# Performance work log

Measured on AMD Instinct MI355X. Metric: run time of the kernel, lower is better.

Reference implementation:

```python
import jax, jax.numpy as jnp
import numpy as np

B, S, V, D = 64, 1024, 1024, 512


def setup_inputs() -> dict:
    key = jax.random.key(0)
    ks = jax.random.split(key, 18)
    sd = 1.0 / np.sqrt(D)
    return dict(
        map_memory=jnp.zeros((B, S, V), jnp.float32),
        step_memory=jnp.zeros((B, S, S), jnp.float32),
        evidence=jax.random.normal(ks[0], (B, D), jnp.float32),
        marker_id=jax.random.randint(ks[1], (B,), 0, 4, jnp.int32),
        source_idx=jax.random.randint(ks[2], (B,), 0, S, jnp.int32),
        source_mask=jax.random.randint(ks[3], (B,), 0, 2, jnp.int32).astype(bool),
        target_symbol_idx=jax.random.randint(ks[4], (B,), 0, S, jnp.int32),
        target_symbol_mask=jax.random.randint(ks[5], (B,), 0, 2, jnp.int32).astype(bool),
        target_value_idx=jax.random.randint(ks[6], (B,), 0, V, jnp.int32),
        target_value_mask=jax.random.randint(ks[7], (B,), 0, 2, jnp.int32).astype(bool),
        map_W1=jax.random.normal(ks[8], (D, D), jnp.float32) * sd,
        map_b1=jnp.zeros((D,), jnp.float32),
        map_W2=jax.random.normal(ks[9], (D, 1), jnp.float32) * sd,
        map_b2=jnp.zeros((1,), jnp.float32),
        step_W1=jax.random.normal(ks[10], (D, D), jnp.float32) * sd,
        step_b1=jnp.zeros((D,), jnp.float32),
        step_W2=jax.random.normal(ks[11], (D, 1), jnp.float32) * sd,
        step_b2=jnp.zeros((1,), jnp.float32),
    )


def _gain(x, W1, b1, W2, b2):
    # Dense -> gelu (flax default: approximate) -> Dense(1)
    h = jax.nn.gelu(x @ W1 + b1)
    return (h @ W2 + b2)[:, 0]  # [B]


def reference(map_memory, step_memory, evidence, marker_id, source_idx,
              source_mask, target_symbol_idx, target_symbol_mask,
              target_value_idx, target_value_mask,
              map_W1, map_b1, map_W2, map_b2,
              step_W1, step_b1, step_W2, step_b2):
    map_gate = jax.nn.sigmoid(_gain(evidence, map_W1, map_b1, map_W2, map_b2))    # [B]
    step_gate = jax.nn.sigmoid(_gain(evidence, step_W1, step_b1, step_W2, step_b2))  # [B]
    map_mask = ((marker_id == 1) | (marker_id == 2)) & source_mask & target_value_mask
    step_mask = (marker_id == 3) & source_mask & target_symbol_mask
    b = jnp.arange(map_memory.shape[0])
    # one-hot outer product 'bs,bv->bsv' * gate is exactly a single gated entry at
    # (source_idx, target_idx) per batch element -> indexed scatter-add.
    next_map = map_memory.at[b, source_idx, target_value_idx].add(
        map_gate * map_mask.astype(map_gate.dtype))
    next_step = step_memory.at[b, source_idx, target_symbol_idx].add(
        step_gate * step_mask.astype(step_gate.dtype))
    return next_map, next_step
```

## Files before the change

### kernel.cpp

```cpp
#include <hip/hip_runtime.h>
#include <math.h>

#define BB 64
#define SS 1024
#define VV 1024
#define DD 512

#define MAP_WORDS  ((size_t)BB * SS * VV)
#define STEP_WORDS ((size_t)BB * SS * SS)
#define TOT_WORDS  (MAP_WORDS + STEP_WORDS)
#define TOT_F4     (TOT_WORDS / 4)
#define MAP_F4     (MAP_WORDS / 4)

#define COPY_BLOCKS 4096
#define COPY_THREADS 256

typedef float f32x4 __attribute__((ext_vector_type(4)));

__device__ __forceinline__ float gelu_tanh(float x) {
    const float k = 0.7978845608028654f;
    float x3 = x * x * x;
    return 0.5f * x * (1.0f + tanhf(k * (x + 0.044715f * x3)));
}

__global__ void __launch_bounds__(COPY_THREADS)
copy_kernel(const f32x4* __restrict__ map_memory,
            const f32x4* __restrict__ step_memory,
            f32x4* __restrict__ out)
{
    const size_t stride = (size_t)COPY_BLOCKS * COPY_THREADS;
    size_t i = (size_t)blockIdx.x * COPY_THREADS + threadIdx.x;
    for (; i < MAP_F4; i += stride) {
        f32x4 v = __builtin_nontemporal_load(&map_memory[i]);
        __builtin_nontemporal_store(v, &out[i]);
    }
    for (i = (size_t)blockIdx.x * COPY_THREADS + threadIdx.x;
         i < (TOT_F4 - MAP_F4); i += stride) {
        f32x4 v = __builtin_nontemporal_load(&step_memory[i]);
        __builtin_nontemporal_store(v, &out[MAP_F4 + i]);
    }
}

__global__ void __launch_bounds__(256)
gate_scatter_kernel(
    const float* __restrict__ evidence,
    const int* __restrict__ marker_id,
    const int* __restrict__ source_idx,
    const int* __restrict__ source_mask,
    const int* __restrict__ target_symbol_idx,
    const int* __restrict__ target_symbol_mask,
    const int* __restrict__ target_value_idx,
    const int* __restrict__ target_value_mask,
    const float* __restrict__ map_W1, const float* __restrict__ map_b1,
    const float* __restrict__ map_W2, const float* __restrict__ map_b2,
    const float* __restrict__ step_W1, const float* __restrict__ step_b1,
    const float* __restrict__ step_W2, const float* __restrict__ step_b2,
    float* __restrict__ out)
{
    const int b    = blockIdx.x >> 1;
    const int head = blockIdx.x & 1;
    const float* W1  = head ? step_W1 : map_W1;
    const float* b1  = head ? step_b1 : map_b1;
    const float* W2  = head ? step_W2 : map_W2;
    const float* b2v = head ? step_b2 : map_b2;

    __shared__ float ev[DD];
    __shared__ float wsum[4];

    const int tid = threadIdx.x;
    for (int i = tid; i < DD; i += 256) ev[i] = evidence[b * DD + i];
    __syncthreads();

    float acc = 0.0f;
    #pragma unroll
    for (int jj = 0; jj < DD; jj += 256) {
        const int j = jj + tid;
        float h = b1[j];
        for (int k = 0; k < DD; ++k) {
            h = fmaf(ev[k], W1[k * DD + j], h);
        }
        h = gelu_tanh(h);
        acc = fmaf(h, W2[j], acc);
    }

    #pragma unroll
    for (int off = 32; off > 0; off >>= 1) acc += __shfl_down(acc, off, 64);
    if ((tid & 63) == 0) wsum[tid >> 6] = acc;
    __syncthreads();

    if (tid == 0) {
        float g = wsum[0] + wsum[1] + wsum[2] + wsum[3] + b2v[0];
        g = 1.0f / (1.0f + expf(-g));
        const int m  = marker_id[b];
        const bool sm = source_mask[b] != 0;
        if (head == 0) {
            if (((m == 1) || (m == 2)) && sm && (target_value_mask[b] != 0)) {
                size_t idx = (size_t)b * SS * VV + (size_t)source_idx[b] * VV
                           + (size_t)target_value_idx[b];
                out[idx] += g;
            }
        } else {
            if ((m == 3) && sm && (target_symbol_mask[b] != 0)) {
                size_t idx = MAP_WORDS + (size_t)b * SS * SS
                           + (size_t)source_idx[b] * SS + (size_t)target_symbol_idx[b];
                out[idx] += g;
            }
        }
    }
}

extern "C" void kernel_launch(void* const* d_in, const int* in_sizes, int n_in,
                              void* d_out, int out_size, void* d_ws, size_t ws_size,
                              hipStream_t stream) {
    const float* map_memory  = (const float*)d_in[0];
    const float* step_memory = (const float*)d_in[1];
    const float* evidence    = (const float*)d_in[2];
    const int* marker_id     = (const int*)d_in[3];
    const int* source_idx    = (const int*)d_in[4];
    const int* source_mask        = (const int*)d_in[5];
    const int* target_symbol_idx  = (const int*)d_in[6];
    const int* target_symbol_mask = (const int*)d_in[7];
    const int* target_value_idx   = (const int*)d_in[8];
    const int* target_value_mask  = (const int*)d_in[9];
    const float* map_W1  = (const float*)d_in[10];
    const float* map_b1  = (const float*)d_in[11];
    const float* map_W2  = (const float*)d_in[12];
    const float* map_b2  = (const float*)d_in[13];
    const float* step_W1 = (const float*)d_in[14];
    const float* step_b1 = (const float*)d_in[15];
    const float* step_W2 = (const float*)d_in[16];
    const float* step_b2 = (const float*)d_in[17];

    float* out = (float*)d_out;

    copy_kernel<<<dim3(COPY_BLOCKS), dim3(COPY_THREADS), 0, stream>>>(
        (const f32x4*)map_memory, (const f32x4*)step_memory, (f32x4*)out);

    gate_scatter_kernel<<<dim3(BB * 2), dim3(256), 0, stream>>>(
        evidence, marker_id, source_idx, source_mask,
        target_symbol_idx, target_symbol_mask,
        target_value_idx, target_value_mask,
        map_W1, map_b1, map_W2, map_b2,
        step_W1, step_b1, step_W2, step_b2,
        out);
}
```

Before: 241.3 us.

## Fuse copy and gate MLP into one launch, defer scatter to tail kernel

After: 256.8 us. +6.4%, slower.

```diff
diff --git a/kernel.cpp b/kernel.cpp
--- a/kernel.cpp
+++ b/kernel.cpp
@@ -12,8 +12,10 @@
 #define TOT_F4     (TOT_WORDS / 4)
 #define MAP_F4     (MAP_WORDS / 4)
 
-#define COPY_BLOCKS 4096
-#define COPY_THREADS 256
+#define COPY_BLOCKS   16384
+#define F4_PER_BLOCK  2048
+#define NGATES        (BB * 2)
+#define TOTAL_BLOCKS  (COPY_BLOCKS + NGATES)
 
 typedef float f32x4 __attribute__((ext_vector_type(4)));
 
@@ -23,26 +25,11 @@
     return 0.5f * x * (1.0f + tanhf(k * (x + 0.044715f * x3)));
 }
 
-__global__ void __launch_bounds__(COPY_THREADS)
-copy_kernel(const f32x4* __restrict__ map_memory,
-            const f32x4* __restrict__ step_memory,
-            f32x4* __restrict__ out)
-{
-    const size_t stride = (size_t)COPY_BLOCKS * COPY_THREADS;
-    size_t i = (size_t)blockIdx.x * COPY_THREADS + threadIdx.x;
-    for (; i < MAP_F4; i += stride) {
-        f32x4 v = __builtin_nontemporal_load(&map_memory[i]);
-        __builtin_nontemporal_store(v, &out[i]);
-    }
-    for (i = (size_t)blockIdx.x * COPY_THREADS + threadIdx.x;
-         i < (TOT_F4 - MAP_F4); i += stride) {
-        f32x4 v = __builtin_nontemporal_load(&step_memory[i]);
-        __builtin_nontemporal_store(v, &out[MAP_F4 + i]);
-    }
-}
-
 __global__ void __launch_bounds__(256)
-gate_scatter_kernel(
+fused_copy_gate_kernel(
+    const f32x4* __restrict__ map_memory,
+    const f32x4* __restrict__ step_memory,
+    f32x4* __restrict__ out,
     const float* __restrict__ evidence,
     const int* __restrict__ marker_id,
     const int* __restrict__ source_idx,
@@ -55,10 +42,37 @@
     const float* __restrict__ map_W2, const float* __restrict__ map_b2,
     const float* __restrict__ step_W1, const float* __restrict__ step_b1,
     const float* __restrict__ step_W2, const float* __restrict__ step_b2,
-    float* __restrict__ out)
+    int* __restrict__ ws_idx, float* __restrict__ ws_g)
 {
-    const int b    = blockIdx.x >> 1;
-    const int head = blockIdx.x & 1;
+    const int blk = blockIdx.x;
+    if (blk < COPY_BLOCKS) {
+        const size_t base = (size_t)blk * F4_PER_BLOCK + threadIdx.x;
+        const f32x4* __restrict__ src =
+            (blk < COPY_BLOCKS / 2) ? (map_memory + base)
+                                    : (step_memory + (base - MAP_F4));
+        f32x4* __restrict__ dst = out + base;
+        f32x4 v0 = src[0 * 256];
+        f32x4 v1 = src[1 * 256];
+        f32x4 v2 = src[2 * 256];
+        f32x4 v3 = src[3 * 256];
+        f32x4 v4 = src[4 * 256];
+        f32x4 v5 = src[5 * 256];
+        f32x4 v6 = src[6 * 256];
+        f32x4 v7 = src[7 * 256];
+        dst[0 * 256] = v0;
+        dst[1 * 256] = v1;
+        dst[2 * 256] = v2;
+        dst[3 * 256] = v3;
+        dst[4 * 256] = v4;
+        dst[5 * 256] = v5;
+        dst[6 * 256] = v6;
+        dst[7 * 256] = v7;
+        return;
+    }
+
+    const int gb   = blk - COPY_BLOCKS;
+    const int b    = gb >> 1;
+    const int head = gb & 1;
     const float* W1  = head ? step_W1 : map_W1;
     const float* b1  = head ? step_b1 : map_b1;
     const float* W2  = head ? step_W2 : map_W2;
@@ -76,6 +90,7 @@
     for (int jj = 0; jj < DD; jj += 256) {
         const int j = jj + tid;
         float h = b1[j];
+        #pragma unroll 8
         for (int k = 0; k < DD; ++k) {
             h = fmaf(ev[k], W1[k * DD + j], h);
         }
@@ -93,20 +108,30 @@
         g = 1.0f / (1.0f + expf(-g));
         const int m  = marker_id[b];
         const bool sm = source_mask[b] != 0;
+        int idx = -1;
         if (head == 0) {
             if (((m == 1) || (m == 2)) && sm && (target_value_mask[b] != 0)) {
-                size_t idx = (size_t)b * SS * VV + (size_t)source_idx[b] * VV
-                           + (size_t)target_value_idx[b];
-                out[idx] += g;
+                idx = b * (SS * VV) + source_idx[b] * VV + target_value_idx[b];
             }
         } else {
             if ((m == 3) && sm && (target_symbol_mask[b] != 0)) {
-                size_t idx = MAP_WORDS + (size_t)b * SS * SS
-                           + (size_t)source_idx[b] * SS + (size_t)target_symbol_idx[b];
-                out[idx] += g;
+                idx = (int)MAP_WORDS + b * (SS * SS) + source_idx[b] * SS
+                    + target_symbol_idx[b];
             }
         }
+        ws_idx[gb] = idx;
+        ws_g[gb]   = g;
     }
+}
+
+__global__ void __launch_bounds__(NGATES)
+scatter_tail_kernel(const int* __restrict__ ws_idx,
+                    const float* __restrict__ ws_g,
+                    float* __restrict__ out)
+{
+    const int i = threadIdx.x;
+    const int idx = ws_idx[i];
+    if (idx >= 0) out[idx] += ws_g[i];
 }
 
 extern "C" void kernel_launch(void* const* d_in, const int* in_sizes, int n_in,
@@ -132,15 +157,18 @@
     const float* step_b2 = (const float*)d_in[17];
 
     float* out = (float*)d_out;
+    char* ws = (char*)d_ws;
+    int*   ws_idx = (int*)ws;
+    float* ws_g   = (float*)(ws + NGATES * sizeof(int));
 
-    copy_kernel<<<dim3(COPY_BLOCKS), dim3(COPY_THREADS), 0, stream>>>(
-        (const f32x4*)map_memory, (const f32x4*)step_memory, (f32x4*)out);
-
-    gate_scatter_kernel<<<dim3(BB * 2), dim3(256), 0, stream>>>(
+    fused_copy_gate_kernel<<<dim3(TOTAL_BLOCKS), dim3(256), 0, stream>>>(
+        (const f32x4*)map_memory, (const f32x4*)step_memory, (f32x4*)out,
         evidence, marker_id, source_idx, source_mask,
         target_symbol_idx, target_symbol_mask,
         target_value_idx, target_value_mask,
         map_W1, map_b1, map_W2, map_b2,
         step_W1, step_b1, step_W2, step_b2,
-        out);
+        ws_idx, ws_g);
+
+    scatter_tail_kernel<<<dim3(1), dim3(NGATES), 0, stream>>>(ws_idx, ws_g, out);
 }
```

## Fuse copy and gated scatter into one kernel, computing gates only in owning blocks

Applied to the files above, without the earlier changes.

After: 247.2 us. 1.02x slower.

```diff
diff --git a/kernel.cpp b/kernel.cpp
--- a/kernel.cpp
+++ b/kernel.cpp
@@ -6,14 +6,15 @@
 #define VV 1024
 #define DD 512
 
-#define MAP_WORDS  ((size_t)BB * SS * VV)
-#define STEP_WORDS ((size_t)BB * SS * SS)
+#define MAP_WORDS  ((long)BB * SS * VV)
+#define STEP_WORDS ((long)BB * SS * SS)
 #define TOT_WORDS  (MAP_WORDS + STEP_WORDS)
 #define TOT_F4     (TOT_WORDS / 4)
 #define MAP_F4     (MAP_WORDS / 4)
 
-#define COPY_BLOCKS 4096
-#define COPY_THREADS 256
+#define THREADS    256
+#define NBLOCKS    ((int)(TOT_F4 / THREADS))
+#define NGATES     (BB * 2)
 
 typedef float f32x4 __attribute__((ext_vector_type(4)));
 
@@ -23,26 +24,11 @@
     return 0.5f * x * (1.0f + tanhf(k * (x + 0.044715f * x3)));
 }
 
-__global__ void __launch_bounds__(COPY_THREADS)
-copy_kernel(const f32x4* __restrict__ map_memory,
-            const f32x4* __restrict__ step_memory,
-            f32x4* __restrict__ out)
-{
-    const size_t stride = (size_t)COPY_BLOCKS * COPY_THREADS;
-    size_t i = (size_t)blockIdx.x * COPY_THREADS + threadIdx.x;
-    for (; i < MAP_F4; i += stride) {
-        f32x4 v = __builtin_nontemporal_load(&map_memory[i]);
-        __builtin_nontemporal_store(v, &out[i]);
-    }
-    for (i = (size_t)blockIdx.x * COPY_THREADS + threadIdx.x;
-         i < (TOT_F4 - MAP_F4); i += stride) {
-        f32x4 v = __builtin_nontemporal_load(&step_memory[i]);
-        __builtin_nontemporal_store(v, &out[MAP_F4 + i]);
-    }
-}
-
-__global__ void __launch_bounds__(256)
-gate_scatter_kernel(
+__global__ void __launch_bounds__(THREADS)
+copy_gate_scatter_kernel(
+    const f32x4* __restrict__ map_memory,
+    const f32x4* __restrict__ step_memory,
+    f32x4* __restrict__ out,
     const float* __restrict__ evidence,
     const int* __restrict__ marker_id,
     const int* __restrict__ source_idx,
@@ -54,59 +40,96 @@
     const float* __restrict__ map_W1, const float* __restrict__ map_b1,
     const float* __restrict__ map_W2, const float* __restrict__ map_b2,
     const float* __restrict__ step_W1, const float* __restrict__ step_b1,
-    const float* __restrict__ step_W2, const float* __restrict__ step_b2,
-    float* __restrict__ out)
+    const float* __restrict__ step_W2, const float* __restrict__ step_b2)
 {
-    const int b    = blockIdx.x >> 1;
-    const int head = blockIdx.x & 1;
-    const float* W1  = head ? step_W1 : map_W1;
-    const float* b1  = head ? step_b1 : map_b1;
-    const float* W2  = head ? step_W2 : map_W2;
-    const float* b2v = head ? step_b2 : map_b2;
+    const int blk = blockIdx.x;
+    const int tid = threadIdx.x;
 
-    __shared__ float ev[DD];
-    __shared__ float wsum[4];
+    __shared__ int nm;
+    __shared__ int m_word[NGATES];
+    __shared__ int m_bh[NGATES];
+    __shared__ float m_g[NGATES];
 
-    const int tid = threadIdx.x;
-    for (int i = tid; i < DD; i += 256) ev[i] = evidence[b * DD + i];
+    if (tid == 0) nm = 0;
     __syncthreads();
 
-    float acc = 0.0f;
-    #pragma unroll
-    for (int jj = 0; jj < DD; jj += 256) {
-        const int j = jj + tid;
-        float h = b1[j];
-        for (int k = 0; k < DD; ++k) {
-            h = fmaf(ev[k], W1[k * DD + j], h);
+    if (tid < NGATES) {
+        const int b = tid >> 1, head = tid & 1;
+        const int m = marker_id[b];
+        const bool sm = source_mask[b] != 0;
+        long idx = -1;
+        if (head == 0) {
+            if (((m == 1) || (m == 2)) && sm && (target_value_mask[b] != 0))
+                idx = (long)b * (SS * VV) + (long)source_idx[b] * VV
+                    + target_value_idx[b];
+        } else {
+            if ((m == 3) && sm && (target_symbol_mask[b] != 0))
+                idx = MAP_WORDS + (long)b * (SS * SS)
+                    + (long)source_idx[b] * SS + target_symbol_idx[b];
         }
-        h = gelu_tanh(h);
-        acc = fmaf(h, W2[j], acc);
+        if (idx >= 0 && (int)(idx >> 10) == blk) {
+            int slot = atomicAdd(&nm, 1);
+            m_word[slot] = (int)(idx & 1023);
+            m_bh[slot]   = tid;
+        }
+    }
+    __syncthreads();
+    const int nmatch = nm;
+
+    if (nmatch) {
+        __shared__ float ev[DD];
+        __shared__ float wsum[4];
+        for (int e = 0; e < nmatch; ++e) {
+            const int bh = m_bh[e];
+            const int b = bh >> 1, head = bh & 1;
+            const float* W1  = head ? step_W1 : map_W1;
+            const float* b1  = head ? step_b1 : map_b1;
+            const float* W2  = head ? step_W2 : map_W2;
+            const float* b2v = head ? step_b2 : map_b2;
+
+            for (int i = tid; i < DD; i += THREADS) ev[i] = evidence[b * DD + i];
+            __syncthreads();
+
+            float acc = 0.0f;
+            #pragma unroll
+            for (int jj = 0; jj < DD; jj += THREADS) {
+                const int j = jj + tid;
+                float h = b1[j];
+                #pragma unroll 8
+                for (int k = 0; k < DD; ++k)
+                    h = fmaf(ev[k], W1[k * DD + j], h);
+                h = gelu_tanh(h);
+                acc = fmaf(h, W2[j], acc);
+            }
+            #pragma unroll
+            for (int off = 32; off > 0; off >>= 1)
+                acc += __shfl_down(acc, off, 64);
+            if ((tid & 63) == 0) wsum[tid >> 6] = acc;
+            __syncthreads();
+            if (tid == 0) {
+                float g = wsum[0] + wsum[1] + wsum[2] + wsum[3] + b2v[0];
+                m_g[e] = 1.0f / (1.0f + expf(-g));
+            }
+            __syncthreads();
+        }
     }
 
-    #pragma unroll
-    for (int off = 32; off > 0; off >>= 1) acc += __shfl_down(acc, off, 64);
-    if ((tid & 63) == 0) wsum[tid >> 6] = acc;
-    __syncthreads();
-
-    if (tid == 0) {
-        float g = wsum[0] + wsum[1] + wsum[2] + wsum[3] + b2v[0];
-        g = 1.0f / (1.0f + expf(-g));
-        const int m  = marker_id[b];
-        const bool sm = source_mask[b] != 0;
-        if (head == 0) {
-            if (((m == 1) || (m == 2)) && sm && (target_value_mask[b] != 0)) {
-                size_t idx = (size_t)b * SS * VV + (size_t)source_idx[b] * VV
-                           + (size_t)target_value_idx[b];
-                out[idx] += g;
-            }
-        } else {
-            if ((m == 3) && sm && (target_symbol_mask[b] != 0)) {
-                size_t idx = MAP_WORDS + (size_t)b * SS * SS
-                           + (size_t)source_idx[b] * SS + (size_t)target_symbol_idx[b];
-                out[idx] += g;
+    const long f4 = (long)blk * THREADS + tid;
+    f32x4 v = (blk < NBLOCKS / 2) ? map_memory[f4]
+                                  : step_memory[f4 - MAP_F4];
+    if (nmatch) {
+        for (int e = 0; e < nmatch; ++e) {
+            if ((m_word[e] >> 2) == tid) {
+                const int ln = m_word[e] & 3;
+                const float g = m_g[e];
+                v.x += (ln == 0) ? g : 0.0f;
+                v.y += (ln == 1) ? g : 0.0f;
+                v.z += (ln == 2) ? g : 0.0f;
+                v.w += (ln == 3) ? g : 0.0f;
             }
         }
     }
+    out[f4] = v;
 }
 
 extern "C" void kernel_launch(void* const* d_in, const int* in_sizes, int n_in,
@@ -131,16 +154,11 @@
     const float* step_W2 = (const float*)d_in[16];
     const float* step_b2 = (const float*)d_in[17];
 
-    float* out = (float*)d_out;
-
-    copy_kernel<<<dim3(COPY_BLOCKS), dim3(COPY_THREADS), 0, stream>>>(
-        (const f32x4*)map_memory, (const f32x4*)step_memory, (f32x4*)out);
-
-    gate_scatter_kernel<<<dim3(BB * 2), dim3(256), 0, stream>>>(
+    copy_gate_scatter_kernel<<<dim3(NBLOCKS), dim3(THREADS), 0, stream>>>(
+        (const f32x4*)map_memory, (const f32x4*)step_memory, (f32x4*)d_out,
         evidence, marker_id, source_idx, source_mask,
         target_symbol_idx, target_symbol_mask,
         target_value_idx, target_value_mask,
         map_W1, map_b1, map_W2, map_b2,
-        step_W1, step_b1, step_W2, step_b2,
-        out);
+        step_W1, step_b1, step_W2, step_b2);
 }
```
